# Performance work log

Measured on AMD Instinct MI355X. Metric: run time of the kernel, lower is better.

The kernel has to match this reference:

```python
import jax, jax.numpy as jnp
import numpy as np

D_MODEL = 1024
N_HEADS = 16
D_KEY = 64
EPS = 1e-5


def setup_inputs() -> dict:
    key = jax.random.key(0)
    ks = jax.random.split(key, 12)
    d, h, dk = D_MODEL, N_HEADS, D_KEY
    s = lambda fan_in: 1.0 / np.sqrt(fan_in)
    inp = {
        "X": jax.random.normal(ks[0], (2, 2048, d), dtype=jnp.float32),
        "Wqkv": jax.random.uniform(ks[1], (d, 3 * h * dk), jnp.float32, -s(d), s(d)),
        "bqkv": jax.random.uniform(ks[2], (3 * h * dk,), jnp.float32, -s(d), s(d)),
        "Wo": jax.random.uniform(ks[3], (h * dk, d), jnp.float32, -s(h * dk), s(h * dk)),
        "bo": jax.random.uniform(ks[4], (d,), jnp.float32, -s(h * dk), s(h * dk)),
        "W1": jax.random.uniform(ks[5], (d, 4 * d), jnp.float32, -s(d), s(d)),
        "b1": jax.random.uniform(ks[6], (4 * d,), jnp.float32, -s(d), s(d)),
        "W2": jax.random.uniform(ks[7], (4 * d, d), jnp.float32, -s(4 * d), s(4 * d)),
        "b2": jax.random.uniform(ks[8], (d,), jnp.float32, -s(4 * d), s(4 * d)),
        "ln1_g": jnp.ones((d,), jnp.float32),
        "ln1_b": jnp.zeros((d,), jnp.float32),
        "ln2_g": jnp.ones((d,), jnp.float32),
        "ln2_b": jnp.zeros((d,), jnp.float32),
    }
    return inp


def _layernorm(x, g, b):
    mu = jnp.mean(x, axis=-1, keepdims=True)
    var = jnp.var(x, axis=-1, keepdims=True)
    return (x - mu) * jax.lax.rsqrt(var + EPS) * g + b


def _block(X, Wqkv, bqkv, Wo, bo, W1, b1, W2, b2, ln1_g, ln1_b, ln2_g, ln2_b):
    B, T, _ = X.shape
    h, dk = N_HEADS, D_KEY
    # --- causal multi-head self-attention on LN(X) ---
    Xn = _layernorm(X, ln1_g, ln1_b)
    qkv = (Xn @ Wqkv + bqkv).reshape(B, T, 3, h, dk)
    q, k, v = (jnp.moveaxis(qkv, 2, 0)[i].transpose(0, 2, 1, 3) for i in range(3))  # each [B,h,T,dk]
    scores = jnp.einsum("bhqd,bhkd->bhqk", q, k) / np.sqrt(dk).astype(np.float32)
    causal = jnp.tril(jnp.ones((T, T), dtype=bool))
    scores = jnp.where(causal, scores, -jnp.inf)
    attn = jax.nn.softmax(scores, axis=-1)
    ctx = jnp.einsum("bhqk,bhkd->bhqd", attn, v)  # [B,h,T,dk]
    ctx = ctx.transpose(0, 2, 1, 3).reshape(B, T, h * dk)
    atten = ctx @ Wo + bo
    X = X + atten  # dropout is identity in eval mode
    # --- FFN on LN(X) ---
    Xn2 = _layernorm(X, ln2_g, ln2_b)
    ffn = jax.nn.relu(Xn2 @ W1 + b1) @ W2 + b2
    return X + ffn


def reference(X, Wqkv, bqkv, Wo, bo, W1, b1, W2, b2, ln1_g, ln1_b, ln2_g, ln2_b):
    return _block(X, Wqkv, bqkv, Wo, bo, W1, b1, W2, b2, ln1_g, ln1_b, ln2_g, ln2_b)
```

## Files before the change

kernel.cpp:

```cpp
#include <hip/hip_runtime.h>
#include <hip/hip_bf16.h>

typedef __hip_bfloat16 bf16;
typedef __attribute__((ext_vector_type(8))) short short8;
typedef __attribute__((ext_vector_type(4))) float f32x4;

constexpr int D     = 1024;
constexpr int T     = 2048;
constexpr int BATCH = 2;
constexpr int ROWS  = BATCH * T;
constexpr int NH    = 16;
constexpr int DKEY  = 64;
constexpr int QKVN  = 3 * D;
constexpr int FFNN  = 4 * D;

static __device__ __forceinline__ float b2f(bf16 x) { return __bfloat162float(x); }
static __device__ __forceinline__ bf16  f2b(float x) { return __float2bfloat16(x); }
static __device__ __forceinline__ float loadf(const bf16* p)  { return __bfloat162float(*p); }
static __device__ __forceinline__ float loadf(const float* p) { return *p; }
static __device__ __forceinline__ float fast_exp2(float x) { return __builtin_amdgcn_exp2f(x); }
static __device__ __forceinline__ unsigned short f2bu(float x) {
    return __bfloat16_as_ushort(__float2bfloat16(x));
}
static __device__ __forceinline__ float us2f(unsigned short u) {
    union { unsigned int i; float f; } c; c.i = ((unsigned int)u) << 16; return c.f;
}

__global__ __launch_bounds__(256) void transpose_cast(const float* __restrict__ in,
                                                      bf16* __restrict__ out,
                                                      int R, int C)
{
    __shared__ float tile[32][33];
    int c0 = blockIdx.x * 32, r0 = blockIdx.y * 32;
    int tx = threadIdx.x & 31, ty = threadIdx.x >> 5;
#pragma unroll
    for (int i = 0; i < 32; i += 8)
        tile[ty + i][tx] = in[(size_t)(r0 + ty + i) * C + c0 + tx];
    __syncthreads();
#pragma unroll
    for (int i = 0; i < 32; i += 8)
        out[(size_t)(c0 + ty + i) * R + r0 + tx] = f2b(tile[tx][ty + i]);
}

template <typename TIN>
__global__ __launch_bounds__(256) void ln_kernel(const TIN* __restrict__ X,
                                                 const float* __restrict__ g,
                                                 const float* __restrict__ b,
                                                 bf16* __restrict__ out)
{
    int row = blockIdx.x;
    int tid = threadIdx.x;
    const TIN* xr = X + (size_t)row * D;
    float v[4];
#pragma unroll
    for (int i = 0; i < 4; ++i) v[i] = loadf(xr + tid + i * 256);

    float s1 = v[0] + v[1] + v[2] + v[3];
    float s2 = v[0]*v[0] + v[1]*v[1] + v[2]*v[2] + v[3]*v[3];
#pragma unroll
    for (int off = 32; off; off >>= 1) {
        s1 += __shfl_xor(s1, off);
        s2 += __shfl_xor(s2, off);
    }
    __shared__ float red[8];
    int lane = tid & 63, w = tid >> 6;
    if (lane == 0) { red[w] = s1; red[4 + w] = s2; }
    __syncthreads();
    s1 = red[0] + red[1] + red[2] + red[3];
    s2 = red[4] + red[5] + red[6] + red[7];

    float mu   = s1 * (1.0f / D);
    float var  = s2 * (1.0f / D) - mu * mu;
    float rstd = rsqrtf(var + 1e-5f);

    bf16* orow = out + (size_t)row * D;
#pragma unroll
    for (int i = 0; i < 4; ++i) {
        int c = tid + i * 256;
        orow[c] = f2b((v[i] - mu) * rstd * g[c] + b[c]);
    }
}

template <int BM, int RELU, int RES, int OUTF32>
__global__ __launch_bounds__(256) void mfma_gemm(
    const bf16* __restrict__ A, const bf16* __restrict__ Bt,
    const float* __restrict__ bias, const void* __restrict__ resid,
    void* __restrict__ out, int M, int N, int K)
{
    constexpr int LDSK = 40;
    constexpr int MT   = BM / 32;
    __shared__ __align__(16) unsigned short As[2][BM * LDSK];
    __shared__ __align__(16) unsigned short Bs[2][128 * LDSK];

    int tid  = threadIdx.x;
    int m0   = blockIdx.y * BM, n0 = blockIdx.x * 128;
    int lane = tid & 63, wave = tid >> 6;
    int wm = (wave >> 1) * (MT * 16), wn = (wave & 1) * 64;
    int c15 = lane & 15, quad = lane >> 4;

    f32x4 acc[MT][4] = {};

    int brow = tid >> 1, bseg = (tid & 1) * 16;
    int arow, aseg;
    if constexpr (BM == 128) { arow = tid >> 1; aseg = (tid & 1) * 16; }
    else                     { arow = tid >> 2; aseg = (tid & 3) * 8;  }
    const bf16* aptr = A  + (size_t)(m0 + arow) * K + aseg;
    const bf16* bptr = Bt + (size_t)(n0 + brow) * K + bseg;

    int nk = K >> 5;
    uint4 ra0, ra1, rb0, rb1;
    ra0 = *(const uint4*)(aptr);
    if constexpr (BM == 128) ra1 = *(const uint4*)(aptr + 8);
    rb0 = *(const uint4*)(bptr);
    rb1 = *(const uint4*)(bptr + 8);

    for (int kt = 0; kt < nk; ++kt) {
        int buf = kt & 1;
        {
            unsigned short* asl = &As[buf][arow * LDSK + aseg];
            unsigned short* bsl = &Bs[buf][brow * LDSK + bseg];
            *(uint4*)asl = ra0;
            if constexpr (BM == 128) *(uint4*)(asl + 8) = ra1;
            *(uint4*)bsl       = rb0;
            *(uint4*)(bsl + 8) = rb1;
        }
        __syncthreads();
        if (kt + 1 < nk) {
            int ko = (kt + 1) * 32;
            ra0 = *(const uint4*)(aptr + ko);
            if constexpr (BM == 128) ra1 = *(const uint4*)(aptr + ko + 8);
            rb0 = *(const uint4*)(bptr + ko);
            rb1 = *(const uint4*)(bptr + ko + 8);
        }
        short8 af[MT], bfr[4];
#pragma unroll
        for (int t = 0; t < MT; ++t)
            af[t]  = *(const short8*)&As[buf][(wm + t * 16 + c15) * LDSK + quad * 8];
#pragma unroll
        for (int t = 0; t < 4; ++t)
            bfr[t] = *(const short8*)&Bs[buf][(wn + t * 16 + c15) * LDSK + quad * 8];
#pragma unroll
        for (int mt = 0; mt < MT; ++mt)
#pragma unroll
            for (int nt = 0; nt < 4; ++nt)
                acc[mt][nt] = __builtin_amdgcn_mfma_f32_16x16x32_bf16(
                    af[mt], bfr[nt], acc[mt][nt], 0, 0, 0);
    }

#pragma unroll
    for (int mt = 0; mt < MT; ++mt) {
#pragma unroll
        for (int nt = 0; nt < 4; ++nt) {
            f32x4 v4 = acc[mt][nt];
            int gc = n0 + wn + nt * 16 + c15;
            float bb = bias[gc];
#pragma unroll
            for (int r = 0; r < 4; ++r) {
                int gr = m0 + wm + mt * 16 + quad * 4 + r;
                float v = v4[r] + bb;
                if constexpr (RELU) v = fmaxf(v, 0.0f);
                size_t idx = (size_t)gr * N + gc;
                if constexpr (RES == 1) v += b2f(((const bf16*)resid)[idx]);
                if constexpr (RES == 2) v += ((const float*)resid)[idx];
                if constexpr (OUTF32) ((float*)out)[idx] = v;
                else                  ((bf16*)out)[idx] = f2b(v);
            }
        }
    }
}

__global__ __launch_bounds__(256) void mfma_gemm_splitk(
    const bf16* __restrict__ A, const bf16* __restrict__ Bt,
    float* __restrict__ P, int M, int N, int K, int klen)
{
    constexpr int LDSK = 40;
    __shared__ __align__(16) unsigned short As[2][128 * LDSK];
    __shared__ __align__(16) unsigned short Bs[2][128 * LDSK];

    int tid  = threadIdx.x;
    int m0   = blockIdx.y * 128, n0 = blockIdx.x * 128;
    int ks   = blockIdx.z * klen;
    int lane = tid & 63, wave = tid >> 6;
    int wm = (wave >> 1) * 64, wn = (wave & 1) * 64;
    int c15 = lane & 15, quad = lane >> 4;

    f32x4 acc[4][4] = {};

    int srow = tid >> 1, sseg = (tid & 1) * 16;
    const bf16* aptr = A  + (size_t)(m0 + srow) * K + ks + sseg;
    const bf16* bptr = Bt + (size_t)(n0 + srow) * K + ks + sseg;

    int nk = klen >> 5;
    uint4 ra0 = *(const uint4*)(aptr), ra1 = *(const uint4*)(aptr + 8);
    uint4 rb0 = *(const uint4*)(bptr), rb1 = *(const uint4*)(bptr + 8);

    for (int kt = 0; kt < nk; ++kt) {
        int buf = kt & 1;
        {
            unsigned short* asl = &As[buf][srow * LDSK + sseg];
            unsigned short* bsl = &Bs[buf][srow * LDSK + sseg];
            *(uint4*)asl       = ra0;
            *(uint4*)(asl + 8) = ra1;
            *(uint4*)bsl       = rb0;
            *(uint4*)(bsl + 8) = rb1;
        }
        __syncthreads();
        if (kt + 1 < nk) {
            int ko = (kt + 1) * 32;
            ra0 = *(const uint4*)(aptr + ko);
            ra1 = *(const uint4*)(aptr + ko + 8);
            rb0 = *(const uint4*)(bptr + ko);
            rb1 = *(const uint4*)(bptr + ko + 8);
        }
        short8 af[4], bfr[4];
#pragma unroll
        for (int t = 0; t < 4; ++t)
            af[t]  = *(const short8*)&As[buf][(wm + t * 16 + c15) * LDSK + quad * 8];
#pragma unroll
        for (int t = 0; t < 4; ++t)
            bfr[t] = *(const short8*)&Bs[buf][(wn + t * 16 + c15) * LDSK + quad * 8];
#pragma unroll
        for (int mt = 0; mt < 4; ++mt)
#pragma unroll
            for (int nt = 0; nt < 4; ++nt)
                acc[mt][nt] = __builtin_amdgcn_mfma_f32_16x16x32_bf16(
                    af[mt], bfr[nt], acc[mt][nt], 0, 0, 0);
    }

#pragma unroll
    for (int mt = 0; mt < 4; ++mt)
#pragma unroll
        for (int nt = 0; nt < 4; ++nt) {
            int gc = n0 + wn + nt * 16 + c15;
#pragma unroll
            for (int r = 0; r < 4; ++r) {
                int gr = m0 + wm + mt * 16 + quad * 4 + r;
                unsafeAtomicAdd(&P[(size_t)gr * N + gc], acc[mt][nt][r]);
            }
        }
}

__global__ __launch_bounds__(256) void reduce_out(const float* __restrict__ P,
                                                  const bf16* __restrict__ X1,
                                                  const float* __restrict__ bias,
                                                  float* __restrict__ out)
{
    int row = blockIdx.x;
    int c   = threadIdx.x * 4;
    size_t idx = (size_t)row * D + c;
    float4 p = *(const float4*)(P + idx);
    float4 bb = *(const float4*)(bias + c);
    ushort4 x = *(const ushort4*)((const unsigned short*)X1 + idx);
    float4 o;
    o.x = p.x + bb.x + us2f(x.x);
    o.y = p.y + bb.y + us2f(x.y);
    o.z = p.z + bb.z + us2f(x.z);
    o.w = p.w + bb.w + us2f(x.w);
    *(float4*)(out + idx) = o;
}

__global__ __launch_bounds__(256) void flash_attn(const bf16* __restrict__ qkv,
                                                  bf16* __restrict__ ctx)
{
    constexpr int KROW = 72;
    constexpr float CSC = 0.18033688011112042f;
    constexpr float MSH = 12.0f;

    __shared__ __align__(16) unsigned short Qs[128 * KROW];
    __shared__ __align__(16) unsigned short Ks[64 * KROW];
    __shared__ __align__(16) unsigned short Vt[64 * KROW];
    unsigned short* Pt = Qs;

    int bx = blockIdx.x;
    int bh = bx & 31;
    int qi = 15 - (bx >> 5);
    int h  = bh & 15, b = bh >> 4;
    int q0 = qi * 128;

    int tid = threadIdx.x, lane = tid & 63, w = tid >> 6;
    int c15 = lane & 15, quad = lane >> 4;

    const bf16* base = qkv + (size_t)b * T * QKVN;

    {
        int row = tid >> 1, half = tid & 1;
        const bf16* src = base + (size_t)(q0 + row) * QKVN + h * 64 + half * 32;
        unsigned short* dst = &Qs[row * KROW + half * 32];
        uint4 v0 = *(const uint4*)(src);
        uint4 v1 = *(const uint4*)(src + 8);
        uint4 v2 = *(const uint4*)(src + 16);
        uint4 v3 = *(const uint4*)(src + 24);
        *(uint4*)(dst)      = v0;
        *(uint4*)(dst + 8)  = v1;
        *(uint4*)(dst + 16) = v2;
        *(uint4*)(dst + 24) = v3;
    }
    __syncthreads();

    short8 qf[2][2];
#pragma unroll
    for (int qt = 0; qt < 2; ++qt)
#pragma unroll
        for (int s = 0; s < 2; ++s)
            qf[qt][s] = *(const short8*)&Qs[(w * 32 + qt * 16 + c15) * KROW + s * 32 + quad * 8];

    short8 ones;
#pragma unroll
    for (int i = 0; i < 8; ++i) ones[i] = (short)0x3F80;

    f32x4 Ot[4][2] = {};
    f32x4 lacc[2]  = {};

    int nkt   = q0 / 64 + 2;
    int wqmin = q0 + w * 32;
    int wqmax = wqmin + 31;

    for (int kt = 0; kt < nkt; ++kt) {
        int k0 = kt * 64;
        int key = tid >> 2, seg = tid & 3;
        const bf16* ksrc = base + (size_t)(k0 + key) * QKVN + D + h * 64 + seg * 16;
        uint4 kv0 = *(const uint4*)ksrc;
        uint4 kv1 = *(const uint4*)(ksrc + 8);
        int keyp = (tid & 31) * 2, dk0 = (tid >> 5) * 8;
        const bf16* vsrc = base + (size_t)(k0 + keyp) * QKVN + 2 * D + h * 64 + dk0;
        uint4 vv0 = *(const uint4*)vsrc;
        uint4 vv1 = *(const uint4*)(vsrc + QKVN);

        __syncthreads();
        {
            unsigned short* kd = &Ks[key * KROW + seg * 16];
            *(uint4*)kd       = kv0;
            *(uint4*)(kd + 8) = kv1;
            const unsigned short* lo = (const unsigned short*)&vv0;
            const unsigned short* hi = (const unsigned short*)&vv1;
#pragma unroll
            for (int j = 0; j < 8; ++j) {
                unsigned int pk = (unsigned int)lo[j] | ((unsigned int)hi[j] << 16);
                *(unsigned int*)&Vt[(dk0 + j) * KROW + keyp] = pk;
            }
        }
        __syncthreads();

        if (k0 <= wqmax) {
            f32x4 St[4][2] = {};
#pragma unroll
            for (int s = 0; s < 2; ++s)
#pragma unroll
                for (int ktm = 0; ktm < 4; ++ktm) {
                    short8 kf = *(const short8*)&Ks[(ktm * 16 + c15) * KROW + s * 32 + quad * 8];
#pragma unroll
                    for (int qt = 0; qt < 2; ++qt)
                        St[ktm][qt] = __builtin_amdgcn_mfma_f32_16x16x32_bf16(
                            kf, qf[qt][s], St[ktm][qt], 0, 0, 0);
                }

            bool diag = (k0 + 63 > wqmin);
#pragma unroll
            for (int ktm = 0; ktm < 4; ++ktm)
#pragma unroll
                for (int qt = 0; qt < 2; ++qt) {
                    ushort4 pk;
                    int q_g = wqmin + qt * 16 + c15;
#pragma unroll
                    for (int r = 0; r < 4; ++r) {
                        float p = fast_exp2(fmaf(St[ktm][qt][r], CSC, -MSH));
                        if (diag && (k0 + ktm * 16 + quad * 4 + r > q_g)) p = 0.0f;
                        ((unsigned short*)&pk)[r] = f2bu(p);
                    }
                    *(ushort4*)&Pt[(w * 32 + qt * 16 + c15) * KROW + ktm * 16 + quad * 4] = pk;
                }

#pragma unroll
            for (int s = 0; s < 2; ++s) {
                short8 pf[2];
#pragma unroll
                for (int qt = 0; qt < 2; ++qt)
                    pf[qt] = *(const short8*)&Pt[(w * 32 + qt * 16 + c15) * KROW + s * 32 + quad * 8];
#pragma unroll
                for (int qt = 0; qt < 2; ++qt)
                    lacc[qt] = __builtin_amdgcn_mfma_f32_16x16x32_bf16(ones, pf[qt], lacc[qt], 0, 0, 0);
#pragma unroll
                for (int dt = 0; dt < 4; ++dt) {
                    short8 vf = *(const short8*)&Vt[(dt * 16 + c15) * KROW + s * 32 + quad * 8];
#pragma unroll
                    for (int qt = 0; qt < 2; ++qt)
                        Ot[dt][qt] = __builtin_amdgcn_mfma_f32_16x16x32_bf16(
                            vf, pf[qt], Ot[dt][qt], 0, 0, 0);
                }
            }
        }
    }

#pragma unroll
    for (int qt = 0; qt < 2; ++qt) {
        float inv = 1.0f / lacc[qt][0];
        int grow = b * T + q0 + w * 32 + qt * 16 + c15;
        bf16* dst = ctx + (size_t)grow * D + h * 64 + quad * 4;
#pragma unroll
        for (int dt = 0; dt < 4; ++dt) {
            ushort4 pk;
#pragma unroll
            for (int r = 0; r < 4; ++r)
                ((unsigned short*)&pk)[r] = f2bu(Ot[dt][qt][r] * inv);
            *(ushort4*)(dst + dt * 16) = pk;
        }
    }
}

extern "C" void kernel_launch(void* const* d_in, const int* in_sizes, int n_in,
                              void* d_out, int out_size, void* d_ws, size_t ws_size,
                              hipStream_t stream)
{
    const float* X    = (const float*)d_in[0];
    const float* Wqkv = (const float*)d_in[1];
    const float* bqkv = (const float*)d_in[2];
    const float* Wo   = (const float*)d_in[3];
    const float* bo   = (const float*)d_in[4];
    const float* W1   = (const float*)d_in[5];
    const float* b1   = (const float*)d_in[6];
    const float* W2   = (const float*)d_in[7];
    const float* b2   = (const float*)d_in[8];
    const float* ln1g = (const float*)d_in[9];
    const float* ln1b = (const float*)d_in[10];
    const float* ln2g = (const float*)d_in[11];
    const float* ln2b = (const float*)d_in[12];
    float* out = (float*)d_out;

    char* ws = (char*)d_ws;
    bf16*  Wqkv_t = (bf16*)(ws + 0);
    bf16*  Wo_t   = (bf16*)(ws + 6291456);
    bf16*  W1_t   = (bf16*)(ws + 8388608);
    bf16*  W2_t   = (bf16*)(ws + 16777216);
    bf16*  Xn     = (bf16*)(ws + 25165824);
    bf16*  X1     = Xn;
    bf16*  Xn2    = (bf16*)(ws + 33554432);
    bf16*  qkv    = (bf16*)(ws + 41943040);
    bf16*  ctx    = (bf16*)(ws + 67108864);
    bf16*  mid    = (bf16*)(ws + 41943040);
    float* P0     = (float*)(ws + 0);

    transpose_cast<<<dim3(QKVN / 32, D / 32), 256, 0, stream>>>(Wqkv, Wqkv_t, D, QKVN);
    transpose_cast<<<dim3(D / 32, D / 32), 256, 0, stream>>>(Wo, Wo_t, D, D);
    transpose_cast<<<dim3(FFNN / 32, D / 32), 256, 0, stream>>>(W1, W1_t, D, FFNN);
    transpose_cast<<<dim3(D / 32, FFNN / 32), 256, 0, stream>>>(W2, W2_t, FFNN, D);

    ln_kernel<float><<<ROWS, 256, 0, stream>>>(X, ln1g, ln1b, Xn);
    mfma_gemm<128, 0, 0, 0><<<dim3(QKVN / 128, ROWS / 128), 256, 0, stream>>>(
        Xn, Wqkv_t, bqkv, nullptr, qkv, ROWS, QKVN, D);
    flash_attn<<<512, 256, 0, stream>>>(qkv, ctx);
    mfma_gemm<64, 0, 2, 0><<<dim3(D / 128, ROWS / 64), 256, 0, stream>>>(
        ctx, Wo_t, bo, X, X1, ROWS, D, D);
    ln_kernel<bf16><<<ROWS, 256, 0, stream>>>(X1, ln2g, ln2b, Xn2);
    mfma_gemm<128, 1, 0, 0><<<dim3(FFNN / 128, ROWS / 128), 256, 0, stream>>>(
        Xn2, W1_t, b1, nullptr, mid, ROWS, FFNN, D);
    hipMemsetAsync(P0, 0, (size_t)ROWS * D * sizeof(float), stream);
    mfma_gemm_splitk<<<dim3(D / 128, ROWS / 128, 2), 256, 0, stream>>>(
        mid, W2_t, P0, ROWS, D, FFNN, FFNN / 2);
    reduce_out<<<ROWS, 256, 0, stream>>>(P0, X1, b2, out);
}
```

Before: 385.4 us.

## Stage GEMM tiles with direct global-to-LDS loads instead of register prefetch

Replaces register-staged, double-buffered LDS tile loading in both GEMM kernels with direct global_load_lds transfers into a single unpadded LDS buffer. This removes the VGPR round trip and halves LDS use, which may raise occupancy. In exchange it loses the overlap between next-tile loads and current MFMA work, adds a second barrier per K step, and drops the row padding, which risks LDS bank conflicts.

```diff
diff --git a/kernel.cpp b/kernel.cpp
--- a/kernel.cpp
+++ b/kernel.cpp
@@ -25,6 +25,11 @@
 static __device__ __forceinline__ float us2f(unsigned short u) {
     union { unsigned int i; float f; } c; c.i = ((unsigned int)u) << 16; return c.f;
 }
+static __device__ __forceinline__ void gl2lds16(const bf16* g, unsigned short* l) {
+    __builtin_amdgcn_global_load_lds(
+        (__attribute__((address_space(1))) void*)g,
+        (__attribute__((address_space(3))) void*)l, 16, 0, 0);
+}
 
 __global__ __launch_bounds__(256) void transpose_cast(const float* __restrict__ in,
                                                       bf16* __restrict__ out,
@@ -87,10 +92,9 @@
     const float* __restrict__ bias, const void* __restrict__ resid,
     void* __restrict__ out, int M, int N, int K)
 {
-    constexpr int LDSK = 40;
-    constexpr int MT   = BM / 32;
-    __shared__ __align__(16) unsigned short As[2][BM * LDSK];
-    __shared__ __align__(16) unsigned short Bs[2][128 * LDSK];
+    constexpr int MT = BM / 32;
+    __shared__ __align__(16) unsigned short As[BM * 32];
+    __shared__ __align__(16) unsigned short Bs[128 * 32];
 
     int tid  = threadIdx.x;
     int m0   = blockIdx.y * BM, n0 = blockIdx.x * 128;
@@ -100,51 +104,39 @@
 
     f32x4 acc[MT][4] = {};
 
-    int brow = tid >> 1, bseg = (tid & 1) * 16;
-    int arow, aseg;
-    if constexpr (BM == 128) { arow = tid >> 1; aseg = (tid & 1) * 16; }
-    else                     { arow = tid >> 2; aseg = (tid & 3) * 8;  }
-    const bf16* aptr = A  + (size_t)(m0 + arow) * K + aseg;
-    const bf16* bptr = Bt + (size_t)(n0 + brow) * K + bseg;
+    int srow = tid >> 2, sseg = (tid & 3) * 8;
+    const bf16* ap0 = A  + (size_t)(m0 + srow) * K + sseg;
+    const bf16* ap1 = ap0 + (size_t)64 * K;
+    const bf16* bp0 = Bt + (size_t)(n0 + srow) * K + sseg;
+    const bf16* bp1 = bp0 + (size_t)64 * K;
+    unsigned short* al0 = &As[tid * 8];
+    unsigned short* al1 = &As[tid * 8 + 2048];
+    unsigned short* bl0 = &Bs[tid * 8];
+    unsigned short* bl1 = &Bs[tid * 8 + 2048];
 
     int nk = K >> 5;
-    uint4 ra0, ra1, rb0, rb1;
-    ra0 = *(const uint4*)(aptr);
-    if constexpr (BM == 128) ra1 = *(const uint4*)(aptr + 8);
-    rb0 = *(const uint4*)(bptr);
-    rb1 = *(const uint4*)(bptr + 8);
-
     for (int kt = 0; kt < nk; ++kt) {
-        int buf = kt & 1;
-        {
-            unsigned short* asl = &As[buf][arow * LDSK + aseg];
-            unsigned short* bsl = &Bs[buf][brow * LDSK + bseg];
-            *(uint4*)asl = ra0;
-            if constexpr (BM == 128) *(uint4*)(asl + 8) = ra1;
-            *(uint4*)bsl       = rb0;
-            *(uint4*)(bsl + 8) = rb1;
-        }
-        __syncthreads();
-        if (kt + 1 < nk) {
-            int ko = (kt + 1) * 32;
-            ra0 = *(const uint4*)(aptr + ko);
-            if constexpr (BM == 128) ra1 = *(const uint4*)(aptr + ko + 8);
-            rb0 = *(const uint4*)(bptr + ko);
-            rb1 = *(const uint4*)(bptr + ko + 8);
-        }
+        int ko = kt * 32;
+        gl2lds16(ap0 + ko, al0);
+        if constexpr (BM == 128) gl2lds16(ap1 + ko, al1);
+        gl2lds16(bp0 + ko, bl0);
+        gl2lds16(bp1 + ko, bl1);
+        __syncthreads();
+
         short8 af[MT], bfr[4];
 #pragma unroll
         for (int t = 0; t < MT; ++t)
-            af[t]  = *(const short8*)&As[buf][(wm + t * 16 + c15) * LDSK + quad * 8];
+            af[t]  = *(const short8*)&As[(wm + t * 16 + c15) * 32 + quad * 8];
 #pragma unroll
         for (int t = 0; t < 4; ++t)
-            bfr[t] = *(const short8*)&Bs[buf][(wn + t * 16 + c15) * LDSK + quad * 8];
+            bfr[t] = *(const short8*)&Bs[(wn + t * 16 + c15) * 32 + quad * 8];
 #pragma unroll
         for (int mt = 0; mt < MT; ++mt)
 #pragma unroll
             for (int nt = 0; nt < 4; ++nt)
                 acc[mt][nt] = __builtin_amdgcn_mfma_f32_16x16x32_bf16(
                     af[mt], bfr[nt], acc[mt][nt], 0, 0, 0);
+        __syncthreads();
     }
 
 #pragma unroll
@@ -173,9 +165,8 @@
     const bf16* __restrict__ A, const bf16* __restrict__ Bt,
     float* __restrict__ P, int M, int N, int K, int klen)
 {
-    constexpr int LDSK = 40;
-    __shared__ __align__(16) unsigned short As[2][128 * LDSK];
-    __shared__ __align__(16) unsigned short Bs[2][128 * LDSK];
+    __shared__ __align__(16) unsigned short As[128 * 32];
+    __shared__ __align__(16) unsigned short Bs[128 * 32];
 
     int tid  = threadIdx.x;
     int m0   = blockIdx.y * 128, n0 = blockIdx.x * 128;
@@ -186,45 +177,39 @@
 
     f32x4 acc[4][4] = {};
 
-    int srow = tid >> 1, sseg = (tid & 1) * 16;
-    const bf16* aptr = A  + (size_t)(m0 + srow) * K + ks + sseg;
-    const bf16* bptr = Bt + (size_t)(n0 + srow) * K + ks + sseg;
+    int srow = tid >> 2, sseg = (tid & 3) * 8;
+    const bf16* ap0 = A  + (size_t)(m0 + srow) * K + ks + sseg;
+    const bf16* ap1 = ap0 + (size_t)64 * K;
+    const bf16* bp0 = Bt + (size_t)(n0 + srow) * K + ks + sseg;
+    const bf16* bp1 = bp0 + (size_t)64 * K;
+    unsigned short* al0 = &As[tid * 8];
+    unsigned short* al1 = &As[tid * 8 + 2048];
+    unsigned short* bl0 = &Bs[tid * 8];
+    unsigned short* bl1 = &Bs[tid * 8 + 2048];
 
     int nk = klen >> 5;
-    uint4 ra0 = *(const uint4*)(aptr), ra1 = *(const uint4*)(aptr + 8);
-    uint4 rb0 = *(const uint4*)(bptr), rb1 = *(const uint4*)(bptr + 8);
-
     for (int kt = 0; kt < nk; ++kt) {
-        int buf = kt & 1;
-        {
-            unsigned short* asl = &As[buf][srow * LDSK + sseg];
-            unsigned short* bsl = &Bs[buf][srow * LDSK + sseg];
-            *(uint4*)asl       = ra0;
-            *(uint4*)(asl + 8) = ra1;
-            *(uint4*)bsl       = rb0;
-            *(uint4*)(bsl + 8) = rb1;
-        }
-        __syncthreads();
-        if (kt + 1 < nk) {
-            int ko = (kt + 1) * 32;
-            ra0 = *(const uint4*)(aptr + ko);
-            ra1 = *(const uint4*)(aptr + ko + 8);
-            rb0 = *(const uint4*)(bptr + ko);
-            rb1 = *(const uint4*)(bptr + ko + 8);
-        }
+        int ko = kt * 32;
+        gl2lds16(ap0 + ko, al0);
+        gl2lds16(ap1 + ko, al1);
+        gl2lds16(bp0 + ko, bl0);
+        gl2lds16(bp1 + ko, bl1);
+        __syncthreads();
+
         short8 af[4], bfr[4];
 #pragma unroll
         for (int t = 0; t < 4; ++t)
-            af[t]  = *(const short8*)&As[buf][(wm + t * 16 + c15) * LDSK + quad * 8];
+            af[t]  = *(const short8*)&As[(wm + t * 16 + c15) * 32 + quad * 8];
 #pragma unroll
         for (int t = 0; t < 4; ++t)
-            bfr[t] = *(const short8*)&Bs[buf][(wn + t * 16 + c15) * LDSK + quad * 8];
+            bfr[t] = *(const short8*)&Bs[(wn + t * 16 + c15) * 32 + quad * 8];
 #pragma unroll
         for (int mt = 0; mt < 4; ++mt)
 #pragma unroll
             for (int nt = 0; nt < 4; ++nt)
                 acc[mt][nt] = __builtin_amdgcn_mfma_f32_16x16x32_bf16(
                     af[mt], bfr[nt], acc[mt][nt], 0, 0, 0);
+        __syncthreads();
     }
 
 #pragma unroll
```

Measured after the change: 398.7 us. +3.5%, slower.
